# Optimization experiments

Hardware: AMD Instinct MI355X
Metric: run time of the kernel (lower is better)

Reference implementation:

```python
import jax, jax.numpy as jnp
import numpy as np

DIM = 1024
T = 16384
WINDOW = 32
DIM_HEAD = 64
HEADS = DIM // DIM_HEAD  # 16
EPS = 1e-5


def setup_inputs() -> dict:
    key = jax.random.key(0)
    k1, k2, k3 = jax.random.split(key, 3)
    x = jax.random.normal(k1, (DIM, T), dtype=jnp.float32)
    w_qkv = jax.random.normal(k2, (3 * DIM, DIM), dtype=jnp.float32) / np.float32(np.sqrt(DIM))
    w_out = jax.random.normal(k3, (DIM, DIM), dtype=jnp.float32) / np.float32(np.sqrt(DIM))
    gamma = jnp.ones((DIM,), dtype=jnp.float32)
    beta = jnp.zeros((DIM,), dtype=jnp.float32)
    return {"x": x, "w_qkv": w_qkv, "w_out": w_out, "gamma": gamma, "beta": beta}


def _rotate_half(t):
    # original: split channels into (2, d/2), swap halves with negation
    d = t.shape[-1]
    return jnp.concatenate((-t[..., d // 2:], t[..., :d // 2]), axis=-1)


def reference(x, w_qkv, w_out, gamma, beta):
    C, Tn = x.shape
    xt = x.T  # (T, C)
    # LayerNorm over channel dim (eqx.nn.LayerNorm, eps=1e-5)
    mu = jnp.mean(xt, axis=-1, keepdims=True)
    var = jnp.var(xt, axis=-1, keepdims=True)
    normed = (xt - mu) * jax.lax.rsqrt(var + EPS) * gamma + beta
    # QKV projection (Linear with weight (out,in), no bias)
    qkv = normed @ w_qkv.T  # (T, 3C)
    q, k, v = jnp.split(qkv, 3, axis=-1)
    w = Tn // WINDOW
    def towin(t):  # (w n) (h d) -> h w n d
        return t.reshape(w, WINDOW, HEADS, DIM_HEAD).transpose(2, 0, 1, 3)
    q, k, v = map(towin, (q, k, v))
    # rotary pos emb over window positions (use_xpos=False -> scale == 1)
    inv_freq = 1.0 / (10000.0 ** (jnp.arange(0, DIM_HEAD, 2, dtype=jnp.float32) / DIM_HEAD))
    tpos = jnp.arange(WINDOW, dtype=jnp.float32)
    freqs = jnp.einsum('i,j->ij', tpos, inv_freq)  # (n, d/2)
    freqs = jnp.concatenate((freqs, freqs), axis=-1)  # (n, d)
    cos, sin = jnp.cos(freqs), jnp.sin(freqs)
    q = q * cos + _rotate_half(q) * sin
    k = k * cos + _rotate_half(k) * sin
    # per-head, per-window full (non-causal) attention
    scale = DIM_HEAD ** -0.5
    logits = jnp.einsum('hwnd,hwmd->hwnm', q, k) * scale
    attn = jax.nn.softmax(logits, axis=-1)
    out = jnp.einsum('hwnm,hwmd->hwnd', attn, v)
    out = out.transpose(1, 2, 0, 3).reshape(Tn, C)  # h w n d -> (w n) (h d)
    out = out @ w_out.T
    return out.T + x
```

## Files before the change

### kernel.cpp

```cpp
#include <hip/hip_runtime.h>

#define T_TOK 16384
#define C_DIM 1024

typedef float f32x4 __attribute__((ext_vector_type(4)));
typedef float f32x16 __attribute__((ext_vector_type(16)));
typedef __bf16 bf16x8 __attribute__((ext_vector_type(8)));
typedef unsigned short u16x8 __attribute__((ext_vector_type(8)));
typedef unsigned short u16x4 __attribute__((ext_vector_type(4)));

__device__ __forceinline__ unsigned short f2bf(float f) {
  union { float f; unsigned u; } v; v.f = f;
  unsigned r = v.u + 0x7fffu + ((v.u >> 16) & 1u);
  return (unsigned short)(r >> 16);
}
__device__ __forceinline__ float bf2f(unsigned short h) {
  union { unsigned u; float f; } v; v.u = ((unsigned)h) << 16;
  return v.f;
}
__device__ __forceinline__ unsigned pk2(float a, float b) {
  return (unsigned)f2bf(a) | ((unsigned)f2bf(b) << 16);
}

__global__ __launch_bounds__(256) void cvt_kernel(const float* __restrict__ in,
                                                  unsigned short* __restrict__ out, int n4) {
  int i = blockIdx.x * 256 + threadIdx.x;
  if (i >= n4) return;
  f32x4 v = *(const f32x4*)(in + (size_t)i * 4);
  u16x4 o;
#pragma unroll
  for (int j = 0; j < 4; ++j) o[j] = f2bf(v[j]);
  *(u16x4*)(out + (size_t)i * 4) = o;
}

__global__ __launch_bounds__(256) void rope_tab_kernel(float* __restrict__ tab) {
  int idx = blockIdx.x * 256 + threadIdx.x;
  if (idx >= 1024) return;
  int mm = idx >> 5, d = idx & 31;
  float invf = powf(10000.f, -(float)d * (1.f / 32.f));
  float ang = (float)mm * invf;
  float s, c;
  sincosf(ang, &s, &c);
  tab[idx * 2] = c;
  tab[idx * 2 + 1] = s;
}

__global__ __launch_bounds__(256) void ln_stats_kernel(const float* __restrict__ x,
                                                       float* __restrict__ mu,
                                                       float* __restrict__ rstd) {
  __shared__ float s1[4][64];
  __shared__ float s2[4][64];
  const int tid = threadIdx.x;
  const int lt = tid & 63, cq = tid >> 6;
  const int t = blockIdx.x * 64 + lt;
  float s = 0.f, ss = 0.f;
  const float* p = x + (size_t)cq * 256 * T_TOK + t;
  for (int c = 0; c < 256; ++c) {
    float v = p[(size_t)c * T_TOK];
    s += v; ss += v * v;
  }
  s1[cq][lt] = s; s2[cq][lt] = ss;
  __syncthreads();
  if (tid < 64) {
    float S  = s1[0][tid] + s1[1][tid] + s1[2][tid] + s1[3][tid];
    float SS = s2[0][tid] + s2[1][tid] + s2[2][tid] + s2[3][tid];
    float m = S * (1.f / 1024.f);
    float var = SS * (1.f / 1024.f) - m * m;
    mu[blockIdx.x * 64 + tid] = m;
    rstd[blockIdx.x * 64 + tid] = rsqrtf(var + 1e-5f);
  }
}

__global__ __launch_bounds__(256) void ln_tr_kernel(const float* __restrict__ x,
                                                    const float* __restrict__ mu,
                                                    const float* __restrict__ rstd,
                                                    const float* __restrict__ gamma,
                                                    const float* __restrict__ beta,
                                                    unsigned short* __restrict__ normed) {
  __shared__ float tile[64][65];
  __shared__ float gs[64], bs[64], ms[64], rs[64];
  const int tid = threadIdx.x;
  const int bt = blockIdx.x & 255;
  const int bc = blockIdx.x >> 8;
  const int t0 = bt * 64, c0 = bc * 64;
  if (tid < 64) {
    gs[tid] = gamma[c0 + tid];
    bs[tid] = beta[c0 + tid];
    ms[tid] = mu[t0 + tid];
    rs[tid] = rstd[t0 + tid];
  }
  const int lc = tid >> 4;
  const int lt4 = (tid & 15) * 4;
#pragma unroll
  for (int r = 0; r < 4; ++r) {
    int c = r * 16 + lc;
    f32x4 v = *(const f32x4*)&x[(size_t)(c0 + c) * T_TOK + t0 + lt4];
    tile[c][lt4 + 0] = v[0]; tile[c][lt4 + 1] = v[1];
    tile[c][lt4 + 2] = v[2]; tile[c][lt4 + 3] = v[3];
  }
  __syncthreads();
#pragma unroll
  for (int r = 0; r < 2; ++r) {
    int idx = r * 256 + tid;
    int t = idx >> 3;
    int c8 = (idx & 7) * 8;
    float m = ms[t], rr = rs[t];
    u16x8 o;
#pragma unroll
    for (int j = 0; j < 8; ++j) {
      float v = tile[c8 + j][t];
      v = (v - m) * rr * gs[c8 + j] + bs[c8 + j];
      o[j] = f2bf(v);
    }
    *(u16x8*)&normed[(size_t)(t0 + t) * C_DIM + c0 + c8] = o;
  }
}

#define GLDS(gp, lp) \
  __builtin_amdgcn_global_load_lds((const __attribute__((address_space(1))) void*)(gp), \
                                   (__attribute__((address_space(3))) void*)(lp), 16, 0, 0)

#define BARF() do { __builtin_amdgcn_s_barrier(); asm volatile("" ::: "memory"); } while (0)
#define VMC(n) asm volatile("s_waitcnt vmcnt(" #n ")" ::: "memory")

template <int EPI>
__global__ __launch_bounds__(512, 2) void gemm8p_kernel(const unsigned short* __restrict__ A,
                                                        const unsigned short* __restrict__ B,
                                                        unsigned short* __restrict__ Obf,
                                                        int ldo, int nbn, int K,
                                                        const float* __restrict__ Xadd,
                                                        float* __restrict__ Ofp) {
  __shared__ unsigned short Lds[2][2][2][8192];
  const int tid = threadIdx.x;
  const int w = tid >> 6, lane = tid & 63;
  const int wm = w >> 2, wn = w & 3;

  const int nbm = gridDim.x / nbn;
  const int mtpx = nbm >> 3;
  const int xcd = blockIdx.x & 7;
  const int ib = blockIdx.x >> 3;
  const int mt = xcd * mtpx + (ib % mtpx);
  const int nt = ib / mtpx;
  const size_t m0 = (size_t)mt * 256, n0 = (size_t)nt * 256;

  const unsigned short* gA = A + (m0 + (lane >> 3)) * (size_t)K + ((lane & 7) ^ (lane >> 3)) * 8;
  const unsigned short* gB = B + (n0 + (lane >> 3)) * (size_t)K + ((lane & 7) ^ (lane >> 3)) * 8;
  const int wrow = w * 8;

  auto stageA = [&](int b, int h, int kt) {
    const unsigned short* g = gA + (size_t)(h * 128) * K + (size_t)kt * 64;
    GLDS(g + (size_t)wrow * K,        &Lds[0][b][h][wrow * 64]);
    GLDS(g + (size_t)(64 + wrow) * K, &Lds[0][b][h][(64 + wrow) * 64]);
  };
  auto stageB = [&](int b, int h, int kt) {
    const unsigned short* g = gB + (size_t)(h * 128) * K + (size_t)kt * 64;
    GLDS(g + (size_t)wrow * K,        &Lds[1][b][h][wrow * 64]);
    GLDS(g + (size_t)(64 + wrow) * K, &Lds[1][b][h][(64 + wrow) * 64]);
  };

  f32x4 acc[8][4];
#pragma unroll
  for (int i = 0; i < 8; ++i)
#pragma unroll
    for (int j = 0; j < 4; ++j) acc[i][j] = (f32x4){0.f, 0.f, 0.f, 0.f};

  const int KT = K >> 6;
  const int off_r = (lane & 15) * 64;
  const int slot0 = (((lane >> 4) ^ (lane & 7)) * 8);
  const int slot1 = slot0 ^ 32;
  const int boff = (wn & 1) * 4096;

  bf16x8 aLo[4][2], aHi[4][2], bLo[2][2], bHi[2][2];

  stageA(0, 0, 0); stageA(0, 1, 0); stageB(0, 0, 0); stageB(0, 1, 0);
  if (KT > 1) {
    stageB(1, 0, 1); stageB(1, 1, 1); stageA(1, 0, 1); stageA(1, 1, 1);
    VMC(8);
  } else {
    VMC(0);
  }
  BARF();

  int bb = 0;
  for (int t = 0; t < KT; ++t, bb ^= 1) {
    const unsigned short* Ab = &Lds[0][bb][wm][0];
    const unsigned short* Bb = &Lds[1][bb][wn >> 1][boff];

#pragma unroll
    for (int mi = 0; mi < 4; ++mi) {
      aLo[mi][0] = *(const bf16x8*)&Ab[mi * 1024 + off_r + slot0];
      aLo[mi][1] = *(const bf16x8*)&Ab[mi * 1024 + off_r + slot1];
    }
#pragma unroll
    for (int ni = 0; ni < 2; ++ni) {
      bLo[ni][0] = *(const bf16x8*)&Bb[ni * 1024 + off_r + slot0];
      bLo[ni][1] = *(const bf16x8*)&Bb[ni * 1024 + off_r + slot1];
      bHi[ni][0] = *(const bf16x8*)&Bb[(ni + 2) * 1024 + off_r + slot0];
      bHi[ni][1] = *(const bf16x8*)&Bb[(ni + 2) * 1024 + off_r + slot1];
    }

    __builtin_amdgcn_s_setprio(1);
#pragma unroll
    for (int mi = 0; mi < 4; ++mi)
#pragma unroll
      for (int ni = 0; ni < 2; ++ni)
#pragma unroll
        for (int ks = 0; ks < 2; ++ks)
          acc[mi][ni] = __builtin_amdgcn_mfma_f32_16x16x32_bf16(aLo[mi][ks], bLo[ni][ks], acc[mi][ni], 0, 0, 0);
    __builtin_amdgcn_s_setprio(0);

#pragma unroll
    for (int mi = 0; mi < 4; ++mi) {
      aHi[mi][0] = *(const bf16x8*)&Ab[(mi + 4) * 1024 + off_r + slot0];
      aHi[mi][1] = *(const bf16x8*)&Ab[(mi + 4) * 1024 + off_r + slot1];
    }

    __builtin_amdgcn_s_setprio(1);
#pragma unroll
    for (int mi = 0; mi < 4; ++mi)
#pragma unroll
      for (int ni = 0; ni < 2; ++ni)
#pragma unroll
        for (int ks = 0; ks < 2; ++ks)
          acc[mi][ni + 2] = __builtin_amdgcn_mfma_f32_16x16x32_bf16(aLo[mi][ks], bHi[ni][ks], acc[mi][ni + 2], 0, 0, 0);
    __builtin_amdgcn_s_setprio(0);
    BARF();

    if (t + 2 < KT) { stageB(bb, 0, t + 2); stageB(bb, 1, t + 2); }

    __builtin_amdgcn_s_setprio(1);
#pragma unroll
    for (int mi = 0; mi < 4; ++mi)
#pragma unroll
      for (int ni = 0; ni < 2; ++ni)
#pragma unroll
        for (int ks = 0; ks < 2; ++ks)
          acc[mi + 4][ni + 2] = __builtin_amdgcn_mfma_f32_16x16x32_bf16(aHi[mi][ks], bHi[ni][ks], acc[mi + 4][ni + 2], 0, 0, 0);
    __builtin_amdgcn_s_setprio(0);
    BARF();

    if (t + 2 < KT) { stageA(bb, 0, t + 2); stageA(bb, 1, t + 2); }

    __builtin_amdgcn_s_setprio(1);
#pragma unroll
    for (int mi = 0; mi < 4; ++mi)
#pragma unroll
      for (int ni = 0; ni < 2; ++ni)
#pragma unroll
        for (int ks = 0; ks < 2; ++ks)
          acc[mi + 4][ni] = __builtin_amdgcn_mfma_f32_16x16x32_bf16(aHi[mi][ks], bLo[ni][ks], acc[mi + 4][ni], 0, 0, 0);
    __builtin_amdgcn_s_setprio(0);

    if (t + 2 < KT) {
      VMC(8);
    } else {
      VMC(0);
    }
    BARF();
  }

  if (EPI == 0) {
    unsigned short* cw = &Lds[0][0][0][0] + (size_t)w * 8192;
#pragma unroll
    for (int mi = 0; mi < 8; ++mi)
#pragma unroll
      for (int ni = 0; ni < 4; ++ni)
#pragma unroll
        for (int r = 0; r < 4; ++r)
          cw[(mi * 16 + (lane >> 4) * 4 + r) * 64 + ni * 16 + (lane & 15)] = f2bf(acc[mi][ni][r]);
    const size_t gr0 = m0 + wm * 128;
    const size_t gc0 = n0 + wn * 64;
#pragma unroll
    for (int it = 0; it < 16; ++it) {
      int idx = it * 64 + lane;
      int rr = idx >> 3, c8 = (idx & 7) * 8;
      *(u16x8*)&Obf[(gr0 + rr) * (size_t)ldo + gc0 + c8] = *(const u16x8*)&cw[rr * 64 + c8];
    }
  } else {
    const size_t gr0 = m0 + wm * 128 + (lane >> 4) * 4;
    const size_t gc0 = n0 + wn * 64 + (lane & 15);
#pragma unroll
    for (int mi = 0; mi < 8; ++mi) {
      size_t row = gr0 + mi * 16;
#pragma unroll
      for (int ni = 0; ni < 4; ++ni) {
        size_t col = gc0 + ni * 16;
        f32x4 xv = *(const f32x4*)&Xadd[col * T_TOK + row];
        f32x4 o = acc[mi][ni] + xv;
        *(f32x4*)&Ofp[col * T_TOK + row] = o;
      }
    }
  }
}

__global__ __launch_bounds__(256) void attn_kernel(const unsigned short* __restrict__ qkv,
                                                   const float* __restrict__ ropeT,
                                                   unsigned short* __restrict__ aout) {
  __shared__ unsigned short Vt[4][64][32];
  const int tid = threadIdx.x;
  const int wv = tid >> 6;
  const int lane = tid & 63;
  const int m = lane & 31;
  const int hi = lane >> 5;
  const int gw = blockIdx.x * 4 + wv;
  const int w = gw >> 4, h = gw & 15;
  const size_t rowbase = ((size_t)(w * 32 + m)) * 3072 + (size_t)h * 64;
  const unsigned short* qp = qkv + rowbase;

  u16x8 qv[4], kv[4], vv[4];
#pragma unroll
  for (int s = 0; s < 4; ++s) {
    int off = s * 16 + hi * 8;
    qv[s] = *(const u16x8*)(qp + off);
    kv[s] = *(const u16x8*)(qp + 1024 + off);
    vv[s] = *(const u16x8*)(qp + 2048 + off);
  }

#pragma unroll
  for (int s = 0; s < 4; ++s)
#pragma unroll
    for (int j = 0; j < 8; ++j) {
      int d = s * 16 + hi * 8 + j;
      int slot = (((m >> 3) ^ (d ^ (d >> 2))) & 3) * 8 + (m & 7);
      Vt[wv][d][slot] = vv[s][j];
    }

  f32x4 ct[2][4];
  const float* tp = ropeT + (size_t)(m * 32 + hi * 8) * 2;
#pragma unroll
  for (int kp = 0; kp < 2; ++kp)
#pragma unroll
    for (int q = 0; q < 4; ++q)
      ct[kp][q] = *(const f32x4*)(tp + kp * 32 + q * 4);

  union FU { unsigned u[4]; bf16x8 v; };
  bf16x8 qfr[4], kfr[4];
#pragma unroll
  for (int ks = 0; ks < 4; ++ks) {
    const int kp = ks & 1;
    FU fq, fk;
#pragma unroll
    for (int jp = 0; jp < 4; ++jp) {
      float c0 = ct[kp][jp][0], s0 = ct[kp][jp][1];
      float c1 = ct[kp][jp][2], s1 = ct[kp][jp][3];
      float q0 = bf2f(qv[ks][2 * jp]), q1 = bf2f(qv[ks][2 * jp + 1]);
      float k0 = bf2f(kv[ks][2 * jp]), k1 = bf2f(kv[ks][2 * jp + 1]);
      float rq0, rq1, rk0, rk1;
      if (ks < 2) {
        rq0 = -bf2f(qv[ks + 2][2 * jp]); rq1 = -bf2f(qv[ks + 2][2 * jp + 1]);
        rk0 = -bf2f(kv[ks + 2][2 * jp]); rk1 = -bf2f(kv[ks + 2][2 * jp + 1]);
      } else {
        rq0 = bf2f(qv[ks - 2][2 * jp]); rq1 = bf2f(qv[ks - 2][2 * jp + 1]);
        rk0 = bf2f(kv[ks - 2][2 * jp]); rk1 = bf2f(kv[ks - 2][2 * jp + 1]);
      }
      fq.u[jp] = pk2(q0 * c0 + rq0 * s0, q1 * c1 + rq1 * s1);
      fk.u[jp] = pk2(k0 * c0 + rk0 * s0, k1 * c1 + rk1 * s1);
    }
    qfr[ks] = fq.v; kfr[ks] = fk.v;
  }

  f32x16 accS;
#pragma unroll
  for (int i = 0; i < 16; ++i) accS[i] = 0.f;
#pragma unroll
  for (int ks = 0; ks < 4; ++ks)
    accS = __builtin_amdgcn_mfma_f32_32x32x16_bf16(kfr[ks], qfr[ks], accS, 0, 0, 0);

  float p[16];
  float mx = -1e30f;
#pragma unroll
  for (int r = 0; r < 16; ++r) { p[r] = accS[r] * 0.125f; mx = fmaxf(mx, p[r]); }
  mx = fmaxf(mx, __shfl_xor(mx, 32, 64));
  float sum = 0.f;
#pragma unroll
  for (int r = 0; r < 16; ++r) { p[r] = __expf(p[r] - mx); sum += p[r]; }
  sum += __shfl_xor(sum, 32, 64);
  const float inv = 1.f / sum;
#pragma unroll
  for (int r = 0; r < 16; ++r) p[r] *= inv;

  bf16x8 pfr[2];
  {
    FU f0, f1;
    unsigned a0 = hi ? pk2(p[0], p[1]) : pk2(p[4], p[5]);
    unsigned a1 = hi ? pk2(p[2], p[3]) : pk2(p[6], p[7]);
    unsigned b0 = (unsigned)__shfl_xor((int)a0, 32, 64);
    unsigned b1 = (unsigned)__shfl_xor((int)a1, 32, 64);
    if (hi) { f0.u[0] = b0; f0.u[1] = b1; f0.u[2] = pk2(p[4], p[5]); f0.u[3] = pk2(p[6], p[7]); }
    else    { f0.u[0] = pk2(p[0], p[1]); f0.u[1] = pk2(p[2], p[3]); f0.u[2] = b0; f0.u[3] = b1; }
    unsigned a2 = hi ? pk2(p[8], p[9])   : pk2(p[12], p[13]);
    unsigned a3 = hi ? pk2(p[10], p[11]) : pk2(p[14], p[15]);
    unsigned b2 = (unsigned)__shfl_xor((int)a2, 32, 64);
    unsigned b3 = (unsigned)__shfl_xor((int)a3, 32, 64);
    if (hi) { f1.u[0] = b2; f1.u[1] = b3; f1.u[2] = pk2(p[12], p[13]); f1.u[3] = pk2(p[14], p[15]); }
    else    { f1.u[0] = pk2(p[8], p[9]); f1.u[1] = pk2(p[10], p[11]); f1.u[2] = b2; f1.u[3] = b3; }
    pfr[0] = f0.v; pfr[1] = f1.v;
  }

  f32x16 accO[2];
#pragma unroll
  for (int i = 0; i < 16; ++i) { accO[0][i] = 0.f; accO[1][i] = 0.f; }
  const int dl = lane & 31;
#pragma unroll
  for (int dh = 0; dh < 2; ++dh) {
    int d = dh * 32 + dl;
    int sx = (d ^ (d >> 2)) & 3;
#pragma unroll
    for (int ks = 0; ks < 2; ++ks) {
      bf16x8 vf = *(const bf16x8*)&Vt[wv][d][(((2 * ks + hi) ^ sx) & 3) * 8];
      accO[dh] = __builtin_amdgcn_mfma_f32_32x32x16_bf16(pfr[ks], vf, accO[dh], 0, 0, 0);
    }
  }

#pragma unroll
  for (int r = 0; r < 16; ++r) {
    int n = (r & 3) + 8 * (r >> 2) + 4 * hi;
    size_t o = (size_t)(w * 32 + n) * 1024 + h * 64 + dl;
    aout[o] = f2bf(accO[0][r]);
    aout[o + 32] = f2bf(accO[1][r]);
  }
}

extern "C" void kernel_launch(void* const* d_in, const int* in_sizes, int n_in,
                              void* d_out, int out_size, void* d_ws, size_t ws_size,
                              hipStream_t stream) {
  const float* x     = (const float*)d_in[0];
  const float* w_qkv = (const float*)d_in[1];
  const float* w_out = (const float*)d_in[2];
  const float* gamma = (const float*)d_in[3];
  const float* beta  = (const float*)d_in[4];

  char* ws = (char*)d_ws;
  unsigned short* wqkv_bf = (unsigned short*)(ws);
  unsigned short* wout_bf = (unsigned short*)(ws + 6291456);
  float* mu    = (float*)(ws + 8388608);
  float* rstd  = (float*)(ws + 8454144);
  float* ropeT = (float*)(ws + 8519680);
  unsigned short* normed = (unsigned short*)(ws + 8527872);
  unsigned short* qkv    = (unsigned short*)(ws + 42082304);
  unsigned short* aout   = normed;

  cvt_kernel<<<3072, 256, 0, stream>>>(w_qkv, wqkv_bf, 3072 * 1024 / 4);
  cvt_kernel<<<1024, 256, 0, stream>>>(w_out, wout_bf, 1024 * 1024 / 4);
  rope_tab_kernel<<<4, 256, 0, stream>>>(ropeT);
  ln_stats_kernel<<<256, 256, 0, stream>>>(x, mu, rstd);
  ln_tr_kernel<<<4096, 256, 0, stream>>>(x, mu, rstd, gamma, beta, normed);
  gemm8p_kernel<0><<<768, 512, 0, stream>>>(normed, wqkv_bf, qkv, 3072, 12, 1024,
                                            nullptr, nullptr);
  attn_kernel<<<2048, 256, 0, stream>>>(qkv, ropeT, aout);
  gemm8p_kernel<1><<<256, 512, 0, stream>>>(aout, wout_bf, nullptr, 0, 4, 1024,
                                            x, (float*)d_out);
}
```

Baseline: 226.4 us.

## Switch GEMMs to 32x32x16 MFMA and transpose output projection operands

Replaces the 16x16x32 bf16 MFMA tiling with 32x32x16 MFMAs holding 4x2 accumulator blocks per wave, using new LDS fragment addressing. The output projection swaps A and B (weights as rows, activations as columns) so the fp32 epilogue writes along the token dimension, giving coalesced 32-lane stores and residual loads into the channel-major output. Block-to-XCD mapping gains a fallback that distributes N tiles when the M tile count is not a multiple of 8. This cuts MFMA instruction count and LDS fragment reads per tile, at the cost of new fragment indexing and scalar rather than vector epilogue stores.

```diff
diff --git a/kernel.cpp b/kernel.cpp
--- a/kernel.cpp
+++ b/kernel.cpp
@@ -124,7 +124,7 @@
 #define VMC(n) asm volatile("s_waitcnt vmcnt(" #n ")" ::: "memory")
 
 template <int EPI>
-__global__ __launch_bounds__(512, 2) void gemm8p_kernel(const unsigned short* __restrict__ A,
+__global__ __launch_bounds__(512, 2) void gemm32_kernel(const unsigned short* __restrict__ A,
                                                         const unsigned short* __restrict__ B,
                                                         unsigned short* __restrict__ Obf,
                                                         int ldo, int nbn, int K,
@@ -134,13 +134,21 @@
   const int tid = threadIdx.x;
   const int w = tid >> 6, lane = tid & 63;
   const int wm = w >> 2, wn = w & 3;
+  const int l7 = lane & 7, hi5 = lane >> 5;
 
   const int nbm = gridDim.x / nbn;
-  const int mtpx = nbm >> 3;
   const int xcd = blockIdx.x & 7;
   const int ib = blockIdx.x >> 3;
-  const int mt = xcd * mtpx + (ib % mtpx);
-  const int nt = ib / mtpx;
+  int mt, nt;
+  if ((nbm & 7) == 0) {
+    const int mtpx = nbm >> 3;
+    mt = xcd * mtpx + (ib % mtpx);
+    nt = ib / mtpx;
+  } else {
+    const int ntpx = nbn >> 3;
+    nt = xcd * ntpx + (ib % ntpx);
+    mt = ib / ntpx;
+  }
   const size_t m0 = (size_t)mt * 256, n0 = (size_t)nt * 256;
 
   const unsigned short* gA = A + (m0 + (lane >> 3)) * (size_t)K + ((lane & 7) ^ (lane >> 3)) * 8;
@@ -158,19 +166,22 @@
     GLDS(g + (size_t)(64 + wrow) * K, &Lds[1][b][h][(64 + wrow) * 64]);
   };
 
-  f32x4 acc[8][4];
-#pragma unroll
-  for (int i = 0; i < 8; ++i)
-#pragma unroll
-    for (int j = 0; j < 4; ++j) acc[i][j] = (f32x4){0.f, 0.f, 0.f, 0.f};
+  f32x16 acc32[4][2];
+#pragma unroll
+  for (int i = 0; i < 4; ++i)
+#pragma unroll
+    for (int j = 0; j < 2; ++j)
+#pragma unroll
+      for (int e = 0; e < 16; ++e) acc32[i][j][e] = 0.f;
 
   const int KT = K >> 6;
-  const int off_r = (lane & 15) * 64;
-  const int slot0 = (((lane >> 4) ^ (lane & 7)) * 8);
-  const int slot1 = slot0 ^ 32;
+  const int rowA = (lane & 31) * 64;
   const int boff = (wn & 1) * 4096;
-
-  bf16x8 aLo[4][2], aHi[4][2], bLo[2][2], bHi[2][2];
+  int slotj[4];
+#pragma unroll
+  for (int j = 0; j < 4; ++j) slotj[j] = ((((j << 1) | hi5) ^ l7) << 3);
+
+  bf16x8 aF[4][4], bF[2][4];
 
   stageA(0, 0, 0); stageA(0, 1, 0); stageB(0, 0, 0); stageB(0, 1, 0);
   if (KT > 1) {
@@ -187,42 +198,33 @@
     const unsigned short* Bb = &Lds[1][bb][wn >> 1][boff];
 
 #pragma unroll
-    for (int mi = 0; mi < 4; ++mi) {
-      aLo[mi][0] = *(const bf16x8*)&Ab[mi * 1024 + off_r + slot0];
-      aLo[mi][1] = *(const bf16x8*)&Ab[mi * 1024 + off_r + slot1];
-    }
-#pragma unroll
-    for (int ni = 0; ni < 2; ++ni) {
-      bLo[ni][0] = *(const bf16x8*)&Bb[ni * 1024 + off_r + slot0];
-      bLo[ni][1] = *(const bf16x8*)&Bb[ni * 1024 + off_r + slot1];
-      bHi[ni][0] = *(const bf16x8*)&Bb[(ni + 2) * 1024 + off_r + slot0];
-      bHi[ni][1] = *(const bf16x8*)&Bb[(ni + 2) * 1024 + off_r + slot1];
+    for (int j = 0; j < 4; ++j) {
+      aF[0][j] = *(const bf16x8*)&Ab[rowA + slotj[j]];
+      aF[1][j] = *(const bf16x8*)&Ab[2048 + rowA + slotj[j]];
+      bF[0][j] = *(const bf16x8*)&Bb[rowA + slotj[j]];
+      bF[1][j] = *(const bf16x8*)&Bb[2048 + rowA + slotj[j]];
     }
 
     __builtin_amdgcn_s_setprio(1);
 #pragma unroll
-    for (int mi = 0; mi < 4; ++mi)
-#pragma unroll
-      for (int ni = 0; ni < 2; ++ni)
-#pragma unroll
-        for (int ks = 0; ks < 2; ++ks)
-          acc[mi][ni] = __builtin_amdgcn_mfma_f32_16x16x32_bf16(aLo[mi][ks], bLo[ni][ks], acc[mi][ni], 0, 0, 0);
+    for (int mi = 0; mi < 2; ++mi)
+#pragma unroll
+      for (int j = 0; j < 4; ++j)
+        acc32[mi][0] = __builtin_amdgcn_mfma_f32_32x32x16_bf16(aF[mi][j], bF[0][j], acc32[mi][0], 0, 0, 0);
     __builtin_amdgcn_s_setprio(0);
 
 #pragma unroll
-    for (int mi = 0; mi < 4; ++mi) {
-      aHi[mi][0] = *(const bf16x8*)&Ab[(mi + 4) * 1024 + off_r + slot0];
-      aHi[mi][1] = *(const bf16x8*)&Ab[(mi + 4) * 1024 + off_r + slot1];
+    for (int j = 0; j < 4; ++j) {
+      aF[2][j] = *(const bf16x8*)&Ab[4096 + rowA + slotj[j]];
+      aF[3][j] = *(const bf16x8*)&Ab[6144 + rowA + slotj[j]];
     }
 
     __builtin_amdgcn_s_setprio(1);
 #pragma unroll
-    for (int mi = 0; mi < 4; ++mi)
-#pragma unroll
-      for (int ni = 0; ni < 2; ++ni)
-#pragma unroll
-        for (int ks = 0; ks < 2; ++ks)
-          acc[mi][ni + 2] = __builtin_amdgcn_mfma_f32_16x16x32_bf16(aLo[mi][ks], bHi[ni][ks], acc[mi][ni + 2], 0, 0, 0);
+    for (int mi = 0; mi < 2; ++mi)
+#pragma unroll
+      for (int j = 0; j < 4; ++j)
+        acc32[mi][1] = __builtin_amdgcn_mfma_f32_32x32x16_bf16(aF[mi][j], bF[1][j], acc32[mi][1], 0, 0, 0);
     __builtin_amdgcn_s_setprio(0);
     BARF();
 
@@ -230,12 +232,10 @@
 
     __builtin_amdgcn_s_setprio(1);
 #pragma unroll
-    for (int mi = 0; mi < 4; ++mi)
-#pragma unroll
-      for (int ni = 0; ni < 2; ++ni)
-#pragma unroll
-        for (int ks = 0; ks < 2; ++ks)
-          acc[mi + 4][ni + 2] = __builtin_amdgcn_mfma_f32_16x16x32_bf16(aHi[mi][ks], bHi[ni][ks], acc[mi + 4][ni + 2], 0, 0, 0);
+    for (int mi = 2; mi < 4; ++mi)
+#pragma unroll
+      for (int j = 0; j < 4; ++j)
+        acc32[mi][1] = __builtin_amdgcn_mfma_f32_32x32x16_bf16(aF[mi][j], bF[1][j], acc32[mi][1], 0, 0, 0);
     __builtin_amdgcn_s_setprio(0);
     BARF();
 
@@ -243,12 +243,10 @@
 
     __builtin_amdgcn_s_setprio(1);
 #pragma unroll
-    for (int mi = 0; mi < 4; ++mi)
-#pragma unroll
-      for (int ni = 0; ni < 2; ++ni)
-#pragma unroll
-        for (int ks = 0; ks < 2; ++ks)
-          acc[mi + 4][ni] = __builtin_amdgcn_mfma_f32_16x16x32_bf16(aHi[mi][ks], bLo[ni][ks], acc[mi + 4][ni], 0, 0, 0);
+    for (int mi = 2; mi < 4; ++mi)
+#pragma unroll
+      for (int j = 0; j < 4; ++j)
+        acc32[mi][0] = __builtin_amdgcn_mfma_f32_32x32x16_bf16(aF[mi][j], bF[0][j], acc32[mi][0], 0, 0, 0);
     __builtin_amdgcn_s_setprio(0);
 
     if (t + 2 < KT) {
@@ -262,12 +260,15 @@
   if (EPI == 0) {
     unsigned short* cw = &Lds[0][0][0][0] + (size_t)w * 8192;
 #pragma unroll
-    for (int mi = 0; mi < 8; ++mi)
-#pragma unroll
-      for (int ni = 0; ni < 4; ++ni)
-#pragma unroll
-        for (int r = 0; r < 4; ++r)
-          cw[(mi * 16 + (lane >> 4) * 4 + r) * 64 + ni * 16 + (lane & 15)] = f2bf(acc[mi][ni][r]);
+    for (int mi = 0; mi < 4; ++mi)
+#pragma unroll
+      for (int ni = 0; ni < 2; ++ni)
+#pragma unroll
+        for (int r = 0; r < 16; ++r) {
+          int rowl = mi * 32 + (r & 3) + ((r >> 2) << 3) + (hi5 << 2);
+          cw[rowl * 64 + ni * 32 + (lane & 31)] = f2bf(acc32[mi][ni][r]);
+        }
+    asm volatile("s_waitcnt lgkmcnt(0)" ::: "memory");
     const size_t gr0 = m0 + wm * 128;
     const size_t gc0 = n0 + wn * 64;
 #pragma unroll
@@ -277,19 +278,18 @@
       *(u16x8*)&Obf[(gr0 + rr) * (size_t)ldo + gc0 + c8] = *(const u16x8*)&cw[rr * 64 + c8];
     }
   } else {
-    const size_t gr0 = m0 + wm * 128 + (lane >> 4) * 4;
-    const size_t gc0 = n0 + wn * 64 + (lane & 15);
-#pragma unroll
-    for (int mi = 0; mi < 8; ++mi) {
-      size_t row = gr0 + mi * 16;
-#pragma unroll
-      for (int ni = 0; ni < 4; ++ni) {
-        size_t col = gc0 + ni * 16;
-        f32x4 xv = *(const f32x4*)&Xadd[col * T_TOK + row];
-        f32x4 o = acc[mi][ni] + xv;
-        *(f32x4*)&Ofp[col * T_TOK + row] = o;
+    const size_t cbase = m0 + wm * 128;
+    const size_t tbase = n0 + wn * 64 + (lane & 31);
+#pragma unroll
+    for (int mi = 0; mi < 4; ++mi)
+#pragma unroll
+      for (int ni = 0; ni < 2; ++ni)
+#pragma unroll
+      for (int r = 0; r < 16; ++r) {
+        size_t c = cbase + mi * 32 + (r & 3) + ((r >> 2) << 3) + (hi5 << 2);
+        size_t o = c * T_TOK + tbase + ni * 32;
+        Ofp[o] = acc32[mi][ni][r] + Xadd[o];
       }
-    }
   }
 }
 
@@ -445,9 +445,9 @@
   rope_tab_kernel<<<4, 256, 0, stream>>>(ropeT);
   ln_stats_kernel<<<256, 256, 0, stream>>>(x, mu, rstd);
   ln_tr_kernel<<<4096, 256, 0, stream>>>(x, mu, rstd, gamma, beta, normed);
-  gemm8p_kernel<0><<<768, 512, 0, stream>>>(normed, wqkv_bf, qkv, 3072, 12, 1024,
+  gemm32_kernel<0><<<768, 512, 0, stream>>>(normed, wqkv_bf, qkv, 3072, 12, 1024,
                                             nullptr, nullptr);
   attn_kernel<<<2048, 256, 0, stream>>>(qkv, ropeT, aout);
-  gemm8p_kernel<1><<<256, 512, 0, stream>>>(aout, wout_bf, nullptr, 0, 4, 1024,
+  gemm32_kernel<1><<<256, 512, 0, stream>>>(wout_bf, aout, nullptr, 0, 64, 1024,
                                             x, (float*)d_out);
 }
```

New measurement: 244.5 us. 8.0% more time.
